# Kernel optimization log

Hardware: AMD Instinct MI355X
Metric: run time of the kernel (lower is better)

The kernel has to match this reference:

```python
import jax, jax.numpy as jnp
import numpy as np

INPUT_DIM = 1024
EMBED_DIM = 256


def setup_inputs() -> dict:
    key = jax.random.key(0)
    ks = jax.random.split(key, 7)
    s_in = 1.0 / np.sqrt(INPUT_DIM)
    x = jax.random.normal(ks[0], (4, 2048, INPUT_DIM), dtype=jnp.float32)
    Wq = jax.random.uniform(ks[1], (INPUT_DIM, EMBED_DIM), jnp.float32, -s_in, s_in)
    bq = jax.random.uniform(ks[2], (EMBED_DIM,), jnp.float32, -s_in, s_in)
    Wk = jax.random.uniform(ks[3], (INPUT_DIM, EMBED_DIM), jnp.float32, -s_in, s_in)
    bk = jax.random.uniform(ks[4], (EMBED_DIM,), jnp.float32, -s_in, s_in)
    Wv = jax.random.uniform(ks[5], (INPUT_DIM, EMBED_DIM), jnp.float32, -s_in, s_in)
    bv = jax.random.uniform(ks[6], (EMBED_DIM,), jnp.float32, -s_in, s_in)
    return {"x": x, "Wq": Wq, "bq": bq, "Wk": Wk, "bk": bk, "Wv": Wv, "bv": bv}


def reference(x, Wq, bq, Wk, bk, Wv, bv):
    # B,T,C -> single-head attention. NOTE: original multiplies by C**0.5.
    C = x.shape[-1]
    scale = jnp.asarray(C, x.dtype) ** 0.5
    q = jnp.einsum('btc,ce->bte', x, Wq) + bq  # [B,T,E]
    k = jnp.einsum('btc,ce->bte', x, Wk) + bk
    v = jnp.einsum('btc,ce->bte', x, Wv) + bv
    wei = jnp.einsum('bqe,bke->bqk', q, k) * scale  # [B,T,T]
    wei = jax.nn.softmax(wei, axis=-1)
    # dropout p=0.0 (eval): identity
    out = jnp.einsum('bqk,bke->bqe', wei, v)  # [B,T,E]
    return out
```

## Files before the change

### kernel.cpp

```cpp
#include <hip/hip_runtime.h>
#include <math.h>

#define IDIM 1024
#define EDIM 256
#define NB 4
#define NT 2048
#define NROW 8192

typedef __attribute__((ext_vector_type(8))) short short8;
typedef __attribute__((ext_vector_type(4))) float f32x4;

#define MFMA16(A,B,C) __builtin_amdgcn_mfma_f32_16x16x32_bf16(A,B,C,0,0,0)
#define GLD16(gsrc, ldst) __builtin_amdgcn_global_load_lds( \
    (const __attribute__((address_space(1))) unsigned int*)(gsrc), \
    (__attribute__((address_space(3))) unsigned int*)(ldst), 16, 0, 0)

#define WAITV4() asm volatile("s_waitcnt vmcnt(4)" ::: "memory")
#define WAITV0() asm volatile("s_waitcnt vmcnt(0)" ::: "memory")
#define BAR() do { asm volatile("" ::: "memory"); __builtin_amdgcn_s_barrier(); \
                   asm volatile("" ::: "memory"); } while (0)

__device__ __forceinline__ unsigned short f2bf(float x){
    unsigned u = __builtin_bit_cast(unsigned, x);
    u += 0x7fffu + ((u >> 16) & 1u);
    return (unsigned short)(u >> 16);
}
__device__ __forceinline__ float bf2f(unsigned short h){
    unsigned u = ((unsigned)h) << 16;
    return __builtin_bit_cast(float, u);
}

__global__ __launch_bounds__(256) void split_w(
    const float* __restrict__ Wq, const float* __restrict__ Wk, const float* __restrict__ Wv,
    ushort* __restrict__ Wqh, ushort* __restrict__ Wql,
    ushort* __restrict__ Wkh, ushort* __restrict__ Wkl,
    ushort* __restrict__ Wvh)
{
    int u = blockIdx.x * 256 + threadIdx.x;
    int z   = u >> 15;
    int rem = u & 32767;
    int ko  = rem >> 8;
    int e   = rem & 255;
    const float* W = (z == 0) ? Wq : (z == 1) ? Wk : Wv;
    ushort* Oh = (z == 0) ? Wqh : (z == 1) ? Wkh : Wvh;
    ushort* Ol = (z == 0) ? Wql : Wkl;
    union { ushort us[8]; uint4 v; } hi, lo;
    #pragma unroll
    for (int j = 0; j < 8; ++j) {
        float wv = W[(size_t)(ko * 8 + j) * 256 + e];
        unsigned short h = f2bf(wv);
        hi.us[j] = h;
        lo.us[j] = f2bf(wv - bf2f(h));
    }
    *(uint4*)(Oh + (size_t)e * 1024 + ko * 8) = hi.v;
    if (z < 2) *(uint4*)(Ol + (size_t)e * 1024 + ko * 8) = lo.v;
}

__global__ __launch_bounds__(256, 3) void qkv_proj(
    const float* __restrict__ X,
    const ushort* __restrict__ Whq, const ushort* __restrict__ Wlq,
    const ushort* __restrict__ Whk, const ushort* __restrict__ Wlk,
    const ushort* __restrict__ Whv,
    const float* __restrict__ bq, const float* __restrict__ bk, const float* __restrict__ bv,
    ushort* __restrict__ Qh, ushort* __restrict__ Ql,
    ushort* __restrict__ Kh, ushort* __restrict__ Kl,
    ushort* __restrict__ Vt)
{
    __shared__ ushort Ah[259 * 8], Al[259 * 8];
    __shared__ ushort Bh[512 * 8], Bl[512 * 8];

    const int tid = threadIdx.x;
    const int lane = tid & 63, w = tid >> 6;
    const int ln = tid & 15, quad = (tid >> 4) & 3;
    const int z = blockIdx.z;
    const int n0 = blockIdx.x * 128, m0 = blockIdx.y * 64;
    const ushort* Wh = (z == 0) ? Whq : (z == 1) ? Whk : Whv;
    const ushort* Wl = (z == 0) ? Wlq : Wlk;

    f32x4 acc[4][2];
    #pragma unroll
    for (int mi = 0; mi < 4; ++mi)
        #pragma unroll
        for (int ni = 0; ni < 2; ++ni) acc[mi][ni] = (f32x4){0.f, 0.f, 0.f, 0.f};

    const int am = tid >> 2, ak8 = (tid & 3) * 8;
    const float* xp = X + (size_t)(m0 + am) * IDIM + ak8;
    const ushort* bsrc0 = Wh + (size_t)(n0 + lane) * IDIM + w * 8;
    const ushort* bsrc1 = Wh + (size_t)(n0 + 64 + lane) * IDIM + w * 8;
    const ushort* blsrc0 = Wl + (size_t)(n0 + lane) * IDIM + w * 8;
    const ushort* blsrc1 = Wl + (size_t)(n0 + 64 + lane) * IDIM + w * 8;
    ushort* bd0 = Bh + (size_t)(w * 128) * 8;
    ushort* bd1 = Bh + (size_t)(w * 128 + 64) * 8;
    ushort* bld0 = Bl + (size_t)(w * 128) * 8;
    ushort* bld1 = Bl + (size_t)(w * 128 + 64) * 8;

    for (int kk = 0; kk < IDIM; kk += 32) {
        GLD16(bsrc0 + kk, bd0);
        GLD16(bsrc1 + kk, bd1);
        if (z < 2) { GLD16(blsrc0 + kk, bld0); GLD16(blsrc1 + kk, bld1); }
        {
            float4 a0 = *(const float4*)(xp + kk);
            float4 a1 = *(const float4*)(xp + kk + 4);
            float xv[8] = {a0.x, a0.y, a0.z, a0.w, a1.x, a1.y, a1.z, a1.w};
            union { ushort us[8]; uint4 v; } hi, lo;
            #pragma unroll
            for (int j = 0; j < 8; ++j) {
                unsigned short hh = f2bf(xv[j]);
                hi.us[j] = hh;
                lo.us[j] = f2bf(xv[j] - bf2f(hh));
            }
            int unit = (tid & 3) * 65 + am;
            *(uint4*)(Ah + unit * 8) = hi.v;
            if (z < 2) *(uint4*)(Al + unit * 8) = lo.v;
        }
        __syncthreads();

        short8 ah[4], al4[4];
        #pragma unroll
        for (int mi = 0; mi < 4; ++mi) {
            int au = quad * 65 + mi * 16 + ln;
            ah[mi] = *(const short8*)(Ah + au * 8);
            if (z < 2) al4[mi] = *(const short8*)(Al + au * 8);
        }
        #pragma unroll
        for (int ni = 0; ni < 2; ++ni) {
            int bu = quad * 128 + w * 32 + ni * 16 + ln;
            short8 bh = *(const short8*)(Bh + bu * 8);
            if (z < 2) {
                short8 bl = *(const short8*)(Bl + bu * 8);
                #pragma unroll
                for (int mi = 0; mi < 4; ++mi) {
                    acc[mi][ni] = MFMA16(ah[mi], bh, acc[mi][ni]);
                    acc[mi][ni] = MFMA16(ah[mi], bl, acc[mi][ni]);
                    acc[mi][ni] = MFMA16(al4[mi], bh, acc[mi][ni]);
                }
            } else {
                #pragma unroll
                for (int mi = 0; mi < 4; ++mi)
                    acc[mi][ni] = MFMA16(ah[mi], bh, acc[mi][ni]);
            }
        }
        __syncthreads();
    }

    if (z < 2) {
        ushort* OH = (z == 0) ? Qh : Kh;
        ushort* OL = (z == 0) ? Ql : Kl;
        const float* bias = (z == 0) ? bq : bk;
        const float scale = (z == 0) ? 46.16624130844683f : 1.0f;
        #pragma unroll
        for (int ni = 0; ni < 2; ++ni) {
            int col = n0 + w * 32 + ni * 16 + ln;
            float bb = bias[col];
            #pragma unroll
            for (int mi = 0; mi < 4; ++mi)
                #pragma unroll
                for (int r = 0; r < 4; ++r) {
                    int row = m0 + mi * 16 + quad * 4 + r;
                    float v = (acc[mi][ni][r] + bb) * scale;
                    unsigned short hh = f2bf(v);
                    OH[(size_t)row * EDIM + col] = hh;
                    OL[(size_t)row * EDIM + col] = f2bf(v - bf2f(hh));
                }
        }
    } else {
        #pragma unroll
        for (int ni = 0; ni < 2; ++ni) {
            int col = n0 + w * 32 + ni * 16 + ln;
            float bb = bv[col];
            #pragma unroll
            for (int mi = 0; mi < 4; ++mi) {
                int rowb = m0 + mi * 16 + quad * 4;
                union { ushort us[4]; uint2 v; } pk;
                #pragma unroll
                for (int r = 0; r < 4; ++r) pk.us[r] = f2bf(acc[mi][ni][r] + bb);
                *(uint2*)(Vt + (size_t)col * NROW + rowb) = pk.v;
            }
        }
    }
}


__device__ __forceinline__ void stageK(const ushort* __restrict__ Kh,
                                       const ushort* __restrict__ Kl,
                                       ushort* buf, int kv0, int kc0, int w, int lane) {
    size_t rowoff = (size_t)(kv0 + w * 16 + (lane & 15)) * EDIM + (lane >> 4) * 8 + kc0 * 32;
    GLD16(Kh + rowoff,      buf + w * 512);
    GLD16(Kh + rowoff + 32, buf + 2048 + w * 512);
    GLD16(Kl + rowoff,      buf + 4096 + w * 512);
    GLD16(Kl + rowoff + 32, buf + 6144 + w * 512);
}

__device__ __forceinline__ void stageV(const ushort* __restrict__ Vt,
                                       ushort* buf, int kv0, int vs0, int w, int lane) {
    size_t gv = (size_t)(vs0 * 64 + w * 16 + (lane & 15)) * NROW + kv0 + (lane >> 4) * 8;
    GLD16(Vt + gv,      buf + w * 1024);
    GLD16(Vt + gv + 32, buf + w * 1024 + 512);
    GLD16(Vt + gv + (size_t)64 * NROW,      buf + 4096 + w * 1024);
    GLD16(Vt + gv + (size_t)64 * NROW + 32, buf + 4096 + w * 1024 + 512);
}

__global__ __launch_bounds__(256, 2) void attn(
    const ushort* __restrict__ Qh, const ushort* __restrict__ Ql,
    const ushort* __restrict__ Kh, const ushort* __restrict__ Kl,
    const ushort* __restrict__ Vt, ushort* __restrict__ Op, float* __restrict__ mlbuf)
{
    __shared__ ushort KVbuf[3 * 8192];
    __shared__ ushort Pall[4 * 1088];

    const int tid = threadIdx.x;
    const int lane = tid & 63;
    const int ln = tid & 15, quad = (tid >> 4) & 3, w = tid >> 6;
    ushort* Pw = Pall + w * 1088;

    const int id = blockIdx.x;
    const int cls = id & 15;
    const int b = cls >> 2, kvq = cls & 3;
    const int qt = id >> 4;
    const int qrow0w = b * NT + qt * 64 + w * 16;
    const int kvbase = b * NT + kvq * 512;

    short8 qh8[8], ql8[8];
    #pragma unroll
    for (int kc = 0; kc < 8; ++kc) {
        qh8[kc] = *(const short8*)(Qh + (size_t)(qrow0w + ln) * EDIM + kc * 32 + quad * 8);
        ql8[kc] = *(const short8*)(Ql + (size_t)(qrow0w + ln) * EDIM + kc * 32 + quad * 8);
    }

    float m_r[4], l_r[4];
    #pragma unroll
    for (int r = 0; r < 4; ++r) { m_r[r] = -3e38f; l_r[r] = 0.f; }
    f32x4 o[16];
    #pragma unroll
    for (int ni = 0; ni < 16; ++ni) o[ni] = (f32x4){0.f, 0.f, 0.f, 0.f};

    stageK(Kh, Kl, KVbuf + 0 * 8192, kvbase, 0, w, lane);
    stageK(Kh, Kl, KVbuf + 1 * 8192, kvbase, 2, w, lane);

    #pragma unroll 1
    for (int t = 0; t < 8; ++t) {
        const int kv0 = kvbase + t * 64;
        f32x4 s[4];
        #pragma unroll
        for (int ni = 0; ni < 4; ++ni) s[ni] = (f32x4){0.f, 0.f, 0.f, 0.f};

        #pragma unroll
        for (int j = 0; j < 4; ++j) {
            WAITV4();
            BAR();
            if (j < 2)      stageK(Kh, Kl, KVbuf + ((j + 2) % 3) * 8192, kv0, 2 * (j + 2), w, lane);
            else if (j == 2) stageV(Vt, KVbuf + 1 * 8192, kv0, 0, w, lane);
            else             stageV(Vt, KVbuf + 2 * 8192, kv0, 2, w, lane);

            const ushort* bufc = KVbuf + (j % 3) * 8192;
            #pragma unroll
            for (int kk = 0; kk < 2; ++kk) {
                const int kc = j * 2 + kk;
                #pragma unroll
                for (int ni = 0; ni < 4; ++ni) {
                    short8 bh = *(const short8*)(bufc + kk * 2048 + (ni * 64 + quad * 16 + ln) * 8);
                    short8 bl = *(const short8*)(bufc + 4096 + kk * 2048 + (ni * 64 + quad * 16 + ln) * 8);
                    s[ni] = MFMA16(qh8[kc], bh, s[ni]);
                    s[ni] = MFMA16(qh8[kc], bl, s[ni]);
                    s[ni] = MFMA16(ql8[kc], bh, s[ni]);
                }
            }
        }

        float mt[4];
        #pragma unroll
        for (int r = 0; r < 4; ++r)
            mt[r] = fmaxf(fmaxf(s[0][r], s[1][r]), fmaxf(s[2][r], s[3][r]));
        #pragma unroll
        for (int mask = 1; mask < 16; mask <<= 1)
            #pragma unroll
            for (int r = 0; r < 4; ++r)
                mt[r] = fmaxf(mt[r], __shfl_xor(mt[r], mask));
        float alpha[4];
        #pragma unroll
        for (int r = 0; r < 4; ++r) {
            float mn = fmaxf(m_r[r], mt[r]);
            alpha[r] = exp2f(m_r[r] - mn);
            m_r[r] = mn;
        }
        float ls[4] = {0.f, 0.f, 0.f, 0.f};
        #pragma unroll
        for (int ni = 0; ni < 4; ++ni) {
            int colb = ni * 16 + ln;
            #pragma unroll
            for (int r = 0; r < 4; ++r) {
                float p = exp2f(s[ni][r] - m_r[r]);
                ls[r] += p;
                Pw[((colb >> 3) * 17 + quad * 4 + r) * 8 + (colb & 7)] = f2bf(p);
            }
        }
        #pragma unroll
        for (int mask = 1; mask < 16; mask <<= 1)
            #pragma unroll
            for (int r = 0; r < 4; ++r)
                ls[r] += __shfl_xor(ls[r], mask);
        #pragma unroll
        for (int r = 0; r < 4; ++r) l_r[r] = l_r[r] * alpha[r] + ls[r];
        #pragma unroll
        for (int ni = 0; ni < 16; ++ni)
            #pragma unroll
            for (int r = 0; r < 4; ++r) o[ni][r] *= alpha[r];

        short8 apk0 = *(const short8*)(Pw + (quad * 17 + ln) * 8);
        short8 apk1 = *(const short8*)(Pw + ((4 + quad) * 17 + ln) * 8);

        #pragma unroll
        for (int j2 = 0; j2 < 2; ++j2) {
            if (t < 7 || j2 == 0) { WAITV4(); } else { WAITV0(); }
            BAR();
            if (t < 7) {
                if (j2 == 0) stageK(Kh, Kl, KVbuf + 0 * 8192, kv0 + 64, 0, w, lane);
                else         stageK(Kh, Kl, KVbuf + 1 * 8192, kv0 + 64, 2, w, lane);
            }
            const ushort* bufc = KVbuf + (1 + j2) * 8192;
            #pragma unroll
            for (int vv = 0; vv < 2; ++vv) {
                const int vs = j2 * 2 + vv;
                #pragma unroll
                for (int ni = 0; ni < 4; ++ni) {
                    short8 v0 = *(const short8*)(bufc + vv * 4096 + (ni * 128 + quad * 16 + ln) * 8);
                    short8 v1 = *(const short8*)(bufc + vv * 4096 + (ni * 128 + 64 + quad * 16 + ln) * 8);
                    o[vs * 4 + ni] = MFMA16(apk0, v0, o[vs * 4 + ni]);
                    o[vs * 4 + ni] = MFMA16(apk1, v1, o[vs * 4 + ni]);
                }
            }
        }
    }

    const int p = (b * 32 + qt) * 4 + kvq;
    if (ln == 0) {
        #pragma unroll
        for (int r = 0; r < 4; ++r) {
            int row = w * 16 + quad * 4 + r;
            *(float2*)(mlbuf + ((size_t)p * 64 + row) * 2) = make_float2(m_r[r], l_r[r]);
        }
    }
    #pragma unroll
    for (int ni = 0; ni < 16; ++ni)
        #pragma unroll
        for (int r = 0; r < 4; ++r) {
            int row = w * 16 + quad * 4 + r;
            Op[(size_t)p * 16384 + row * 256 + ni * 16 + ln] = f2bf(o[ni][r]);
        }
}

__global__ __launch_bounds__(256) void attn_merge(
    const ushort* __restrict__ Op, const float* __restrict__ mlbuf, float* __restrict__ out)
{
    const int bid = blockIdx.x, t = threadIdx.x;
    const int b = bid >> 7, qt = (bid >> 2) & 31, rg = bid & 3;
    const int row = rg * 16 + (t >> 4);
    const int e0 = (t & 15) * 16;
    const int pb = (b * 32 + qt) * 4;
    float mv[4], lv[4];
    float M = -3e38f;
    #pragma unroll
    for (int w2 = 0; w2 < 4; ++w2) {
        float2 ml = *(const float2*)(mlbuf + ((size_t)(pb + w2) * 64 + row) * 2);
        mv[w2] = ml.x; lv[w2] = ml.y;
        M = fmaxf(M, ml.x);
    }
    float sc[4], denom = 0.f;
    #pragma unroll
    for (int w2 = 0; w2 < 4; ++w2) {
        sc[w2] = exp2f(mv[w2] - M);
        denom += sc[w2] * lv[w2];
    }
    float inv = 1.0f / denom;
    #pragma unroll
    for (int w2 = 0; w2 < 4; ++w2) sc[w2] *= inv;

    float acc[16] = {};
    #pragma unroll
    for (int w2 = 0; w2 < 4; ++w2) {
        const ushort* src = Op + (size_t)(pb + w2) * 16384 + row * 256 + e0;
        #pragma unroll
        for (int c = 0; c < 2; ++c) {
            union { ushort us[8]; uint4 v; } u;
            u.v = *(const uint4*)(src + c * 8);
            #pragma unroll
            for (int j = 0; j < 8; ++j)
                acc[c * 8 + j] += sc[w2] * bf2f(u.us[j]);
        }
    }
    float* op = out + ((size_t)b * NT + qt * 64 + row) * EDIM + e0;
    #pragma unroll
    for (int g = 0; g < 4; ++g)
        *(float4*)(op + g * 4) = make_float4(acc[g*4], acc[g*4+1], acc[g*4+2], acc[g*4+3]);
}

extern "C" void kernel_launch(void* const* d_in, const int* in_sizes, int n_in,
                              void* d_out, int out_size, void* d_ws, size_t ws_size,
                              hipStream_t stream) {
    const float* x  = (const float*)d_in[0];
    const float* Wq = (const float*)d_in[1];
    const float* bq = (const float*)d_in[2];
    const float* Wk = (const float*)d_in[3];
    const float* bk = (const float*)d_in[4];
    const float* Wv = (const float*)d_in[5];
    const float* bv = (const float*)d_in[6];
    float* out = (float*)d_out;

    const size_t NE = (size_t)NB * NT * EDIM;
    ushort* Qh = (ushort*)d_ws;
    ushort* Ql = Qh + NE;
    ushort* Kh = Ql + NE;
    ushort* Kl = Kh + NE;
    ushort* Vt = Kl + NE;
    ushort* Wqh = Vt + NE;
    ushort* Wql = Wqh + 256 * 1024;
    ushort* Wkh = Wql + 256 * 1024;
    ushort* Wkl = Wkh + 256 * 1024;
    ushort* Wvh = Wkl + 256 * 1024;
    ushort* Op  = Wvh + 256 * 1024;
    float*  mlb = (float*)(Op + (size_t)512 * 16384);

    split_w<<<384, 256, 0, stream>>>(Wq, Wk, Wv, Wqh, Wql, Wkh, Wkl, Wvh);
    qkv_proj<<<dim3(2, 128, 3), 256, 0, stream>>>(x, Wqh, Wql, Wkh, Wkl, Wvh,
                                                  bq, bk, bv, Qh, Ql, Kh, Kl, Vt);
    attn<<<512, 256, 0, stream>>>(Qh, Ql, Kh, Kl, Vt, Op, mlb);
    attn_merge<<<512, 256, 0, stream>>>(Op, mlb, out);
}
```

Before: 206.1 us.

## Double-buffer QKV projection LDS, add setprio around MFMA, skip unneeded rescale

The QKV projection now uses double-buffered LDS tiles, so the next K-slice's weight loads and fp32-to-bf16 split of x overlap MFMA work on the current slice. This halves the barriers per K step but doubles shared memory use, which may reduce occupancy. s_setprio raises wave priority around the MFMA blocks in both kernels. In the attention kernel, the online-softmax rescale of the output accumulators and running sum is skipped when no row's max increased anywhere in the wave, saving exp2 calls and 64 multiplies per tile at the cost of a ballot.

```diff
diff --git a/kernel.cpp b/kernel.cpp
--- a/kernel.cpp
+++ b/kernel.cpp
@@ -66,8 +66,8 @@
     ushort* __restrict__ Kh, ushort* __restrict__ Kl,
     ushort* __restrict__ Vt)
 {
-    __shared__ ushort Ah[259 * 8], Al[259 * 8];
-    __shared__ ushort Bh[512 * 8], Bl[512 * 8];
+    __shared__ ushort Ah[2][259 * 8], Al[2][259 * 8];
+    __shared__ ushort Bh[2][512 * 8], Bl[2][512 * 8];
 
     const int tid = threadIdx.x;
     const int lane = tid & 63, w = tid >> 6;
@@ -84,64 +84,75 @@
         for (int ni = 0; ni < 2; ++ni) acc[mi][ni] = (f32x4){0.f, 0.f, 0.f, 0.f};
 
     const int am = tid >> 2, ak8 = (tid & 3) * 8;
+    const int unit = (tid & 3) * 65 + am;
     const float* xp = X + (size_t)(m0 + am) * IDIM + ak8;
     const ushort* bsrc0 = Wh + (size_t)(n0 + lane) * IDIM + w * 8;
     const ushort* bsrc1 = Wh + (size_t)(n0 + 64 + lane) * IDIM + w * 8;
     const ushort* blsrc0 = Wl + (size_t)(n0 + lane) * IDIM + w * 8;
     const ushort* blsrc1 = Wl + (size_t)(n0 + 64 + lane) * IDIM + w * 8;
-    ushort* bd0 = Bh + (size_t)(w * 128) * 8;
-    ushort* bd1 = Bh + (size_t)(w * 128 + 64) * 8;
-    ushort* bld0 = Bl + (size_t)(w * 128) * 8;
-    ushort* bld1 = Bl + (size_t)(w * 128 + 64) * 8;
-
-    for (int kk = 0; kk < IDIM; kk += 32) {
-        GLD16(bsrc0 + kk, bd0);
-        GLD16(bsrc1 + kk, bd1);
-        if (z < 2) { GLD16(blsrc0 + kk, bld0); GLD16(blsrc1 + kk, bld1); }
-        {
-            float4 a0 = *(const float4*)(xp + kk);
-            float4 a1 = *(const float4*)(xp + kk + 4);
-            float xv[8] = {a0.x, a0.y, a0.z, a0.w, a1.x, a1.y, a1.z, a1.w};
-            union { ushort us[8]; uint4 v; } hi, lo;
-            #pragma unroll
-            for (int j = 0; j < 8; ++j) {
-                unsigned short hh = f2bf(xv[j]);
-                hi.us[j] = hh;
-                lo.us[j] = f2bf(xv[j] - bf2f(hh));
-            }
-            int unit = (tid & 3) * 65 + am;
-            *(uint4*)(Ah + unit * 8) = hi.v;
-            if (z < 2) *(uint4*)(Al + unit * 8) = lo.v;
-        }
+
+#define QSTAGE(pb, kk) do { \
+    GLD16(bsrc0 + (kk), Bh[pb] + w * 1024); \
+    GLD16(bsrc1 + (kk), Bh[pb] + w * 1024 + 512); \
+    if (z < 2) { GLD16(blsrc0 + (kk), Bl[pb] + w * 1024); \
+                 GLD16(blsrc1 + (kk), Bl[pb] + w * 1024 + 512); } \
+    float4 a0 = *(const float4*)(xp + (kk)); \
+    float4 a1 = *(const float4*)(xp + (kk) + 4); \
+    float xv[8] = {a0.x, a0.y, a0.z, a0.w, a1.x, a1.y, a1.z, a1.w}; \
+    union { ushort us[8]; uint4 v; } hi, lo; \
+    _Pragma("unroll") \
+    for (int j = 0; j < 8; ++j) { \
+        unsigned short hh = f2bf(xv[j]); \
+        hi.us[j] = hh; \
+        lo.us[j] = f2bf(xv[j] - bf2f(hh)); \
+    } \
+    *(uint4*)(Ah[pb] + unit * 8) = hi.v; \
+    if (z < 2) *(uint4*)(Al[pb] + unit * 8) = lo.v; \
+} while (0)
+
+#define QCOMP(cb) do { \
+    short8 ah[4], al4[4]; \
+    _Pragma("unroll") \
+    for (int mi = 0; mi < 4; ++mi) { \
+        int au = quad * 65 + mi * 16 + ln; \
+        ah[mi] = *(const short8*)(Ah[cb] + au * 8); \
+        if (z < 2) al4[mi] = *(const short8*)(Al[cb] + au * 8); \
+    } \
+    __builtin_amdgcn_s_setprio(1); \
+    _Pragma("unroll") \
+    for (int ni = 0; ni < 2; ++ni) { \
+        int bu = quad * 128 + w * 32 + ni * 16 + ln; \
+        short8 bh = *(const short8*)(Bh[cb] + bu * 8); \
+        if (z < 2) { \
+            short8 bl = *(const short8*)(Bl[cb] + bu * 8); \
+            _Pragma("unroll") \
+            for (int mi = 0; mi < 4; ++mi) { \
+                acc[mi][ni] = MFMA16(ah[mi], bh, acc[mi][ni]); \
+                acc[mi][ni] = MFMA16(ah[mi], bl, acc[mi][ni]); \
+                acc[mi][ni] = MFMA16(al4[mi], bh, acc[mi][ni]); \
+            } \
+        } else { \
+            _Pragma("unroll") \
+            for (int mi = 0; mi < 4; ++mi) \
+                acc[mi][ni] = MFMA16(ah[mi], bh, acc[mi][ni]); \
+        } \
+    } \
+    __builtin_amdgcn_s_setprio(0); \
+} while (0)
+
+    QSTAGE(0, 0);
+    __syncthreads();
+    #pragma unroll 1
+    for (int ks2 = 0; ks2 < 16; ++ks2) {
+        QSTAGE(1, ks2 * 64 + 32);
+        QCOMP(0);
         __syncthreads();
-
-        short8 ah[4], al4[4];
-        #pragma unroll
-        for (int mi = 0; mi < 4; ++mi) {
-            int au = quad * 65 + mi * 16 + ln;
-            ah[mi] = *(const short8*)(Ah + au * 8);
-            if (z < 2) al4[mi] = *(const short8*)(Al + au * 8);
-        }
-        #pragma unroll
-        for (int ni = 0; ni < 2; ++ni) {
-            int bu = quad * 128 + w * 32 + ni * 16 + ln;
-            short8 bh = *(const short8*)(Bh + bu * 8);
-            if (z < 2) {
-                short8 bl = *(const short8*)(Bl + bu * 8);
-                #pragma unroll
-                for (int mi = 0; mi < 4; ++mi) {
-                    acc[mi][ni] = MFMA16(ah[mi], bh, acc[mi][ni]);
-                    acc[mi][ni] = MFMA16(ah[mi], bl, acc[mi][ni]);
-                    acc[mi][ni] = MFMA16(al4[mi], bh, acc[mi][ni]);
-                }
-            } else {
-                #pragma unroll
-                for (int mi = 0; mi < 4; ++mi)
-                    acc[mi][ni] = MFMA16(ah[mi], bh, acc[mi][ni]);
-            }
-        }
+        if (ks2 < 15) QSTAGE(0, ks2 * 64 + 64);
+        QCOMP(1);
         __syncthreads();
     }
+#undef QSTAGE
+#undef QCOMP
 
     if (z < 2) {
         ushort* OH = (z == 0) ? Qh : Kh;
@@ -180,7 +191,6 @@
     }
 }
 
-
 __device__ __forceinline__ void stageK(const ushort* __restrict__ Kh,
                                        const ushort* __restrict__ Kl,
                                        ushort* buf, int kv0, int kc0, int w, int lane) {
@@ -253,6 +263,7 @@
             else             stageV(Vt, KVbuf + 2 * 8192, kv0, 2, w, lane);
 
             const ushort* bufc = KVbuf + (j % 3) * 8192;
+            __builtin_amdgcn_s_setprio(1);
             #pragma unroll
             for (int kk = 0; kk < 2; ++kk) {
                 const int kc = j * 2 + kk;
@@ -265,6 +276,7 @@
                     s[ni] = MFMA16(ql8[kc], bh, s[ni]);
                 }
             }
+            __builtin_amdgcn_s_setprio(0);
         }
 
         float mt[4];
@@ -276,12 +288,22 @@
             #pragma unroll
             for (int r = 0; r < 4; ++r)
                 mt[r] = fmaxf(mt[r], __shfl_xor(mt[r], mask));
-        float alpha[4];
-        #pragma unroll
-        for (int r = 0; r < 4; ++r) {
-            float mn = fmaxf(m_r[r], mt[r]);
-            alpha[r] = exp2f(m_r[r] - mn);
-            m_r[r] = mn;
+        int need = (mt[0] > m_r[0]) || (mt[1] > m_r[1]) ||
+                   (mt[2] > m_r[2]) || (mt[3] > m_r[3]);
+        if (__ballot(need)) {
+            float alpha[4];
+            #pragma unroll
+            for (int r = 0; r < 4; ++r) {
+                float mn = fmaxf(m_r[r], mt[r]);
+                alpha[r] = exp2f(m_r[r] - mn);
+                m_r[r] = mn;
+            }
+            #pragma unroll
+            for (int r = 0; r < 4; ++r) l_r[r] *= alpha[r];
+            #pragma unroll
+            for (int ni = 0; ni < 16; ++ni)
+                #pragma unroll
+                for (int r = 0; r < 4; ++r) o[ni][r] *= alpha[r];
         }
         float ls[4] = {0.f, 0.f, 0.f, 0.f};
         #pragma unroll
@@ -300,11 +322,7 @@
             for (int r = 0; r < 4; ++r)
                 ls[r] += __shfl_xor(ls[r], mask);
         #pragma unroll
-        for (int r = 0; r < 4; ++r) l_r[r] = l_r[r] * alpha[r] + ls[r];
-        #pragma unroll
-        for (int ni = 0; ni < 16; ++ni)
-            #pragma unroll
-            for (int r = 0; r < 4; ++r) o[ni][r] *= alpha[r];
+        for (int r = 0; r < 4; ++r) l_r[r] += ls[r];
 
         short8 apk0 = *(const short8*)(Pw + (quad * 17 + ln) * 8);
         short8 apk1 = *(const short8*)(Pw + ((4 + quad) * 17 + ln) * 8);
@@ -318,6 +336,7 @@
                 else         stageK(Kh, Kl, KVbuf + 1 * 8192, kv0 + 64, 2, w, lane);
             }
             const ushort* bufc = KVbuf + (1 + j2) * 8192;
+            __builtin_amdgcn_s_setprio(1);
             #pragma unroll
             for (int vv = 0; vv < 2; ++vv) {
                 const int vs = j2 * 2 + vv;
@@ -329,6 +348,7 @@
                     o[vs * 4 + ni] = MFMA16(apk1, v1, o[vs * 4 + ni]);
                 }
             }
+            __builtin_amdgcn_s_setprio(0);
         }
     }
 
```

Result: no change. 204.7 us (-0.7%).
